# Performance work log

Measured on AMD Instinct MI355X. Metric: run time of the kernel, lower is better.

## Reference

```python
import jax, jax.numpy as jnp
import numpy as np

T, N, M, B = 512, 512, 256, 256

def setup_inputs() -> dict:
    key = jax.random.key(0)
    ks = jax.random.split(key, 6)
    h_t = jax.random.normal(ks[0], (1, B, M), dtype=jnp.float32)
    s_t = jax.random.normal(ks[1], (1, B, M), dtype=jnp.float32)
    data = jax.random.normal(ks[2], (B, T, N), dtype=jnp.float32)
    # torch Linear weight layout: (out_features, in_features)
    W_e = jax.random.normal(ks[3], (T, 2 * M), dtype=jnp.float32) / np.sqrt(2 * M)
    U_e = jax.random.normal(ks[4], (T, T), dtype=jnp.float32) / np.sqrt(T)
    v_e = jax.random.normal(ks[5], (1, T), dtype=jnp.float32) / np.sqrt(T)
    return {"h_t": h_t, "s_t": s_t, "data": data, "W_e": W_e, "U_e": U_e, "v_e": v_e}

def reference(h_t, s_t, data, W_e, U_e, v_e):
    # h_t, s_t: (1, B, m) -> (B, 2m); query is identical across the n repeats,
    # so project once and broadcast instead of materializing (B, n, 2m).
    query = jnp.concatenate([h_t[0], s_t[0]], axis=-1)          # (B, 2m)
    wq = query @ W_e.T                                          # (B, T)
    ud = jnp.einsum('btn,st->bns', data, U_e)                   # (B, n, T)
    alpha = jnp.tanh(wq[:, None, :] + ud)                       # (B, n, T)
    scores = jnp.einsum('bnt,t->bn', alpha, v_e[0])             # (B, n)
    attn = jax.nn.softmax(scores, axis=-1)[:, None, :]          # (B, 1, n)
    return attn
```

## Files before the change

### kernel.cpp

```cpp
#include <hip/hip_runtime.h>
#include <hip/hip_bf16.h>
#include <cmath>

#define T_DIM 512
#define N_DIM 512
#define M_DIM 256
#define B_DIM 256

typedef __bf16 bf16x8 __attribute__((ext_vector_type(8)));
typedef float  f32x4  __attribute__((ext_vector_type(4)));
typedef unsigned int u32;

__device__ __forceinline__ void gload16(const __bf16* g, __bf16* l) {
    __builtin_amdgcn_global_load_lds(
        (const __attribute__((address_space(1))) void*)g,
        (__attribute__((address_space(3))) void*)l, 16, 0, 0);
}

__device__ __forceinline__ int bkey(int r) { return ((r >> 3) ^ (r >> 1)) & 3; }

__device__ __forceinline__ u32 pack_trunc(float hi, float lo) {
    return __builtin_amdgcn_perm(__builtin_bit_cast(u32, hi),
                                 __builtin_bit_cast(u32, lo), 0x07060302u);
}

__device__ __forceinline__ float ftanh(float x) {
    return 1.f - 2.f / (__expf(2.f * x) + 1.f);
}

__global__ __launch_bounds__(256) void uconv_kernel(
    const float* __restrict__ U, __bf16* __restrict__ Uh)
{
    const int i = (blockIdx.x * 256 + threadIdx.x) * 2;
    float2 v = *(const float2*)(U + i);
    Uh[i]   = (__bf16)v.x;
    Uh[i+1] = (__bf16)v.y;
}

__global__ __launch_bounds__(256) void wq_kernel(
    const float* __restrict__ h_t, const float* __restrict__ s_t,
    const float* __restrict__ W_e, float* __restrict__ wq)
{
    __shared__ float q[2 * M_DIM];
    const int b = blockIdx.x;
    const int tid = threadIdx.x;
    q[tid]         = h_t[(size_t)b * M_DIM + tid];
    q[M_DIM + tid] = s_t[(size_t)b * M_DIM + tid];
    __syncthreads();
    for (int tt = tid; tt < T_DIM; tt += 256) {
        const float4* wrow = (const float4*)(W_e + (size_t)tt * (2 * M_DIM));
        float acc = 0.f;
        #pragma unroll 4
        for (int k4 = 0; k4 < (2 * M_DIM) / 4; ++k4) {
            float4 w = wrow[k4];
            acc += q[4*k4+0] * w.x + q[4*k4+1] * w.y
                 + q[4*k4+2] * w.z + q[4*k4+3] * w.w;
        }
        wq[(size_t)b * T_DIM + tt] = acc;
    }
}

__global__ __launch_bounds__(512, 2) void fused11_kernel(
    const float* __restrict__ data, const __bf16* __restrict__ Uh,
    const float* __restrict__ v_e, const float* __restrict__ wq,
    float* __restrict__ scores)
{
    __shared__ __align__(16) __bf16 As[2][128 * 32];
    __shared__ __align__(16) __bf16 Bs[2][512 * 32];
    __shared__ float sc2[4][128];

    const int wg   = blockIdx.x;
    const int bgrp = wg >> 2;
    const int nb   = wg & 3;

    const int tid  = threadIdx.x;
    const int lane = tid & 63;
    const int wid  = tid >> 6;
    const int wm   = wid >> 2;
    const int wn   = wid & 3;

    f32x4 acc[4][8];
    const f32x4 zero = {0.f, 0.f, 0.f, 0.f};
    #pragma unroll
    for (int i = 0; i < 4; ++i)
        #pragma unroll
        for (int j = 0; j < 8; ++j)
            acc[i][j] = zero;

    const int rp = tid >> 5;
    const int nq = tid & 31;
    const int n0 = nq * 4;

    const float* Apan = data + ((size_t)bgrp * 4 * T_DIM) * N_DIM + nb * 128 + n0;

    const __bf16* Bb = Uh;
    const int r0   = tid >> 2;
    const int keyB = bkey(r0);
    const int ce   = (((tid & 3) ^ keyB) * 8);

    const int fr = lane & 15;
    const int kb = (lane >> 4) * 8;

    int aoff[4];
    #pragma unroll
    for (int mi = 0; mi < 4; ++mi) {
        const int row = wm * 64 + mi * 16 + fr;
        aoff[mi] = row * 32 + (kb ^ (bkey(row) << 3));
    }
    int boff[8];
    #pragma unroll
    for (int ni = 0; ni < 8; ++ni) {
        const int row = wn * 128 + ni * 16 + fr;
        boff[ni] = row * 32 + (kb ^ (bkey(row) << 3));
    }

    float vev[8];
    #pragma unroll
    for (int ni = 0; ni < 8; ++ni)
        vev[ni] = v_e[wn * 128 + ni * 16 + fr];
    const int g = lane >> 4;

    float4 pa0, pa1;
    {
        const float* s0 = Apan + (size_t)(2 * rp) * N_DIM;
        pa0 = *(const float4*)s0;
        pa1 = *(const float4*)(s0 + N_DIM);
    }
    #pragma unroll
    for (int i = 0; i < 4; ++i)
        gload16(Bb + (size_t)(i * 128 + r0) * T_DIM + ce,
                &Bs[0][0] + (size_t)i * 128 * 32 + tid * 8);
    {
        u32* As32 = (u32*)As[0];
        const float lo_[4] = {pa0.x, pa0.y, pa0.z, pa0.w};
        const float hi_[4] = {pa1.x, pa1.y, pa1.z, pa1.w};
        #pragma unroll
        for (int j = 0; j < 4; ++j) {
            const u32 w = pack_trunc(hi_[j], lo_[j]);
            const int key = bkey(n0 + j);
            As32[(n0 + j) * 16 + (rp ^ (key << 2))] = w;
        }
    }
    {
        const float* sn = Apan + (size_t)(32 + 2 * rp) * N_DIM;
        pa0 = *(const float4*)sn;
        pa1 = *(const float4*)(sn + N_DIM);
    }
    __syncthreads();

    for (int t = 0; t < 64; ++t) {
        const int cur = t & 1;

        bf16x8 a[4], bv[8];
        #pragma unroll
        for (int mi = 0; mi < 4; ++mi)
            a[mi] = *(const bf16x8*)&As[cur][aoff[mi]];
        #pragma unroll
        for (int ni = 0; ni < 8; ++ni)
            bv[ni] = *(const bf16x8*)&Bs[cur][boff[ni]];

        if (t < 63) {
            const int nxt = cur ^ 1;
            const int kcol = ((t + 1) & 15) << 5;
            #pragma unroll
            for (int i = 0; i < 4; ++i)
                gload16(Bb + (size_t)(i * 128 + r0) * T_DIM + kcol + ce,
                        &Bs[nxt][0] + (size_t)i * 128 * 32 + tid * 8);
            u32* As32 = (u32*)As[nxt];
            const float lo_[4] = {pa0.x, pa0.y, pa0.z, pa0.w};
            const float hi_[4] = {pa1.x, pa1.y, pa1.z, pa1.w};
            #pragma unroll
            for (int j = 0; j < 4; ++j) {
                const u32 w = pack_trunc(hi_[j], lo_[j]);
                const int key = bkey(n0 + j);
                As32[(n0 + j) * 16 + (rp ^ (key << 2))] = w;
            }
            if (t < 62) {
                const float* sn = Apan + (size_t)(32 * (t + 2) + 2 * rp) * N_DIM;
                pa0 = *(const float4*)sn;
                pa1 = *(const float4*)(sn + N_DIM);
            }
        }

        __builtin_amdgcn_s_setprio(1);
        #pragma unroll
        for (int mi = 0; mi < 4; ++mi)
            #pragma unroll
            for (int ni = 0; ni < 8; ++ni)
                acc[mi][ni] = __builtin_amdgcn_mfma_f32_16x16x32_bf16(a[mi], bv[ni], acc[mi][ni], 0, 0, 0);
        __builtin_amdgcn_s_setprio(0);

        __syncthreads();

        if ((t & 15) == 15) {
            const int b = bgrp * 4 + (t >> 4);
            float wqv[8];
            #pragma unroll
            for (int ni = 0; ni < 8; ++ni)
                wqv[ni] = wq[(size_t)b * T_DIM + wn * 128 + ni * 16 + fr];
            #pragma unroll
            for (int mi = 0; mi < 4; ++mi) {
                #pragma unroll
                for (int rg = 0; rg < 4; ++rg) {
                    float part = 0.f;
                    #pragma unroll
                    for (int ni = 0; ni < 8; ++ni)
                        part += vev[ni] * ftanh(wqv[ni] + acc[mi][ni][rg]);
                    part += __shfl_xor(part, 1);
                    part += __shfl_xor(part, 2);
                    part += __shfl_xor(part, 4);
                    part += __shfl_xor(part, 8);
                    if (fr == 0)
                        sc2[wn][wm * 64 + mi * 16 + 4 * g + rg] = part;
                }
            }
            __syncthreads();
            if (tid < 128) {
                const float s = sc2[0][tid] + sc2[1][tid] + sc2[2][tid] + sc2[3][tid];
                scores[(size_t)b * N_DIM + nb * 128 + tid] = s;
            }
            if (t < 63) {
                #pragma unroll
                for (int i = 0; i < 4; ++i)
                    #pragma unroll
                    for (int j = 0; j < 8; ++j)
                        acc[i][j] = zero;
            }
        }
    }
}

__global__ __launch_bounds__(512) void softmax_kernel(
    const float* __restrict__ scores, float* __restrict__ out)
{
    const int b = blockIdx.x;
    const int n = threadIdx.x;
    float s = scores[(size_t)b * N_DIM + n];

    float m = s;
    #pragma unroll
    for (int off = 1; off < 64; off <<= 1)
        m = fmaxf(m, __shfl_xor(m, off));
    __shared__ float red[8];
    const int wv = n >> 6;
    if ((n & 63) == 0) red[wv] = m;
    __syncthreads();
    float bm = red[0];
    #pragma unroll
    for (int i = 1; i < 8; ++i) bm = fmaxf(bm, red[i]);

    float e = expf(s - bm);
    float t = e;
    #pragma unroll
    for (int off = 1; off < 64; off <<= 1)
        t += __shfl_xor(t, off);
    __syncthreads();
    if ((n & 63) == 0) red[wv] = t;
    __syncthreads();
    float tot = 0.f;
    #pragma unroll
    for (int i = 0; i < 8; ++i) tot += red[i];

    out[(size_t)b * N_DIM + n] = e / tot;
}

extern "C" void kernel_launch(void* const* d_in, const int* in_sizes, int n_in,
                              void* d_out, int out_size, void* d_ws, size_t ws_size,
                              hipStream_t stream) {
    const float* h_t  = (const float*)d_in[0];
    const float* s_t  = (const float*)d_in[1];
    const float* data = (const float*)d_in[2];
    const float* W_e  = (const float*)d_in[3];
    const float* U_e  = (const float*)d_in[4];
    const float* v_e  = (const float*)d_in[5];
    float* out = (float*)d_out;

    const size_t wq_elems     = (size_t)B_DIM * T_DIM;
    const size_t score_elems  = (size_t)B_DIM * N_DIM;
    const size_t u_elems      = (size_t)T_DIM * T_DIM;

    float* wq      = (float*)d_ws;
    float* scores  = wq + wq_elems;
    __bf16* Uh     = (__bf16*)(scores + score_elems);

    wq_kernel<<<B_DIM, 256, 0, stream>>>(h_t, s_t, W_e, wq);
    uconv_kernel<<<(int)(u_elems / 512), 256, 0, stream>>>(U_e, Uh);
    fused11_kernel<<<256, 512, 0, stream>>>(data, Uh, v_e, wq, scores);
    softmax_kernel<<<B_DIM, 512, 0, stream>>>(scores, out);
}
```

Baseline: 162.1 us.

## Triple-buffer U tiles with prefetch distance two and explicit vmcnt waits

```diff
diff --git a/kernel.cpp b/kernel.cpp
--- a/kernel.cpp
+++ b/kernel.cpp
@@ -10,6 +10,11 @@
 typedef __bf16 bf16x8 __attribute__((ext_vector_type(8)));
 typedef float  f32x4  __attribute__((ext_vector_type(4)));
 typedef unsigned int u32;
+
+#define WAITVM(N) asm volatile("s_waitcnt vmcnt(" #N ") lgkmcnt(0)" ::: "memory")
+#define FENCED_BARRIER() do { __builtin_amdgcn_sched_barrier(0); \
+                              __builtin_amdgcn_s_barrier();      \
+                              __builtin_amdgcn_sched_barrier(0); } while (0)
 
 __device__ __forceinline__ void gload16(const __bf16* g, __bf16* l) {
     __builtin_amdgcn_global_load_lds(
@@ -60,13 +65,13 @@
     }
 }
 
-__global__ __launch_bounds__(512, 2) void fused11_kernel(
+__global__ __launch_bounds__(512, 2) void fused12_kernel(
     const float* __restrict__ data, const __bf16* __restrict__ Uh,
     const float* __restrict__ v_e, const float* __restrict__ wq,
     float* __restrict__ scores)
 {
     __shared__ __align__(16) __bf16 As[2][128 * 32];
-    __shared__ __align__(16) __bf16 Bs[2][512 * 32];
+    __shared__ __align__(16) __bf16 Bs[3][512 * 32];
     __shared__ float sc2[4][128];
 
     const int wg   = blockIdx.x;
@@ -90,13 +95,11 @@
     const int rp = tid >> 5;
     const int nq = tid & 31;
     const int n0 = nq * 4;
-
     const float* Apan = data + ((size_t)bgrp * 4 * T_DIM) * N_DIM + nb * 128 + n0;
 
     const __bf16* Bb = Uh;
     const int r0   = tid >> 2;
-    const int keyB = bkey(r0);
-    const int ce   = (((tid & 3) ^ keyB) * 8);
+    const int ce   = (((tid & 3) ^ bkey(r0)) * 8);
 
     const int fr = lane & 15;
     const int kb = (lane >> 4) * 8;
@@ -121,113 +124,127 @@
     const int g = lane >> 4;
 
     float4 pa0, pa1;
-    {
-        const float* s0 = Apan + (size_t)(2 * rp) * N_DIM;
-        pa0 = *(const float4*)s0;
-        pa1 = *(const float4*)(s0 + N_DIM);
-    }
-    #pragma unroll
-    for (int i = 0; i < 4; ++i)
-        gload16(Bb + (size_t)(i * 128 + r0) * T_DIM + ce,
-                &Bs[0][0] + (size_t)i * 128 * 32 + tid * 8);
-    {
-        u32* As32 = (u32*)As[0];
-        const float lo_[4] = {pa0.x, pa0.y, pa0.z, pa0.w};
-        const float hi_[4] = {pa1.x, pa1.y, pa1.z, pa1.w};
-        #pragma unroll
-        for (int j = 0; j < 4; ++j) {
-            const u32 w = pack_trunc(hi_[j], lo_[j]);
-            const int key = bkey(n0 + j);
-            As32[(n0 + j) * 16 + (rp ^ (key << 2))] = w;
-        }
-    }
-    {
-        const float* sn = Apan + (size_t)(32 + 2 * rp) * N_DIM;
-        pa0 = *(const float4*)sn;
-        pa1 = *(const float4*)(sn + N_DIM);
-    }
-    __syncthreads();
-
-    for (int t = 0; t < 64; ++t) {
-        const int cur = t & 1;
-
-        bf16x8 a[4], bv[8];
-        #pragma unroll
-        for (int mi = 0; mi < 4; ++mi)
-            a[mi] = *(const bf16x8*)&As[cur][aoff[mi]];
-        #pragma unroll
-        for (int ni = 0; ni < 8; ++ni)
-            bv[ni] = *(const bf16x8*)&Bs[cur][boff[ni]];
-
-        if (t < 63) {
-            const int nxt = cur ^ 1;
-            const int kcol = ((t + 1) & 15) << 5;
-            #pragma unroll
-            for (int i = 0; i < 4; ++i)
-                gload16(Bb + (size_t)(i * 128 + r0) * T_DIM + kcol + ce,
-                        &Bs[nxt][0] + (size_t)i * 128 * 32 + tid * 8);
-            u32* As32 = (u32*)As[nxt];
-            const float lo_[4] = {pa0.x, pa0.y, pa0.z, pa0.w};
-            const float hi_[4] = {pa1.x, pa1.y, pa1.z, pa1.w};
-            #pragma unroll
-            for (int j = 0; j < 4; ++j) {
-                const u32 w = pack_trunc(hi_[j], lo_[j]);
-                const int key = bkey(n0 + j);
-                As32[(n0 + j) * 16 + (rp ^ (key << 2))] = w;
-            }
-            if (t < 62) {
-                const float* sn = Apan + (size_t)(32 * (t + 2) + 2 * rp) * N_DIM;
-                pa0 = *(const float4*)sn;
-                pa1 = *(const float4*)(sn + N_DIM);
-            }
-        }
-
-        __builtin_amdgcn_s_setprio(1);
-        #pragma unroll
-        for (int mi = 0; mi < 4; ++mi)
-            #pragma unroll
-            for (int ni = 0; ni < 8; ++ni)
-                acc[mi][ni] = __builtin_amdgcn_mfma_f32_16x16x32_bf16(a[mi], bv[ni], acc[mi][ni], 0, 0, 0);
-        __builtin_amdgcn_s_setprio(0);
-
-        __syncthreads();
-
-        if ((t & 15) == 15) {
-            const int b = bgrp * 4 + (t >> 4);
-            float wqv[8];
-            #pragma unroll
-            for (int ni = 0; ni < 8; ++ni)
-                wqv[ni] = wq[(size_t)b * T_DIM + wn * 128 + ni * 16 + fr];
-            #pragma unroll
-            for (int mi = 0; mi < 4; ++mi) {
-                #pragma unroll
-                for (int rg = 0; rg < 4; ++rg) {
-                    float part = 0.f;
-                    #pragma unroll
-                    for (int ni = 0; ni < 8; ++ni)
-                        part += vev[ni] * ftanh(wqv[ni] + acc[mi][ni][rg]);
-                    part += __shfl_xor(part, 1);
-                    part += __shfl_xor(part, 2);
-                    part += __shfl_xor(part, 4);
-                    part += __shfl_xor(part, 8);
-                    if (fr == 0)
-                        sc2[wn][wm * 64 + mi * 16 + 4 * g + rg] = part;
-                }
-            }
-            __syncthreads();
-            if (tid < 128) {
-                const float s = sc2[0][tid] + sc2[1][tid] + sc2[2][tid] + sc2[3][tid];
-                scores[(size_t)b * N_DIM + nb * 128 + tid] = s;
-            }
-            if (t < 63) {
-                #pragma unroll
-                for (int i = 0; i < 4; ++i)
-                    #pragma unroll
-                    for (int j = 0; j < 8; ++j)
-                        acc[i][j] = zero;
-            }
-        }
-    }
+
+#define CVT_STORE(DST)                                                        \
+    {                                                                         \
+        u32* As32_ = (u32*)(DST);                                             \
+        const float lo_[4] = {pa0.x, pa0.y, pa0.z, pa0.w};                    \
+        const float hi_[4] = {pa1.x, pa1.y, pa1.z, pa1.w};                    \
+        _Pragma("unroll")                                                     \
+        for (int j = 0; j < 4; ++j) {                                         \
+            const u32 w_ = pack_trunc(hi_[j], lo_[j]);                        \
+            const int key_ = bkey(n0 + j);                                    \
+            As32_[(n0 + j) * 16 + (rp ^ (key_ << 2))] = w_;                   \
+        }                                                                     \
+    }
+
+#define LOAD_PA(T)                                                            \
+    {                                                                         \
+        const float* sn_ = Apan + (size_t)(32 * (T) + 2 * rp) * N_DIM;        \
+        pa0 = *(const float4*)sn_;                                            \
+        pa1 = *(const float4*)(sn_ + N_DIM);                                  \
+    }
+
+#define STAGE_B(T, RING)                                                      \
+    {                                                                         \
+        const int kcol_ = ((T) & 15) << 5;                                    \
+        _Pragma("unroll")                                                     \
+        for (int i = 0; i < 4; ++i)                                           \
+            gload16(Bb + (size_t)(i * 128 + r0) * T_DIM + kcol_ + ce,         \
+                    &Bs[RING][0] + (size_t)i * 128 * 32 + tid * 8);           \
+    }
+
+#define K_STEP(K, CURA, RINGC, RINGS, MODE)                                   \
+    {                                                                         \
+        bf16x8 a_[4], bv_[8];                                                 \
+        _Pragma("unroll")                                                     \
+        for (int mi = 0; mi < 4; ++mi)                                        \
+            a_[mi] = *(const bf16x8*)&As[CURA][aoff[mi]];                     \
+        _Pragma("unroll")                                                     \
+        for (int ni = 0; ni < 8; ++ni)                                        \
+            bv_[ni] = *(const bf16x8*)&Bs[RINGC][boff[ni]];                   \
+        if ((MODE) <= 1) CVT_STORE(As[(CURA) ^ 1]);                           \
+        if ((MODE) == 0) { LOAD_PA((K) + 2); STAGE_B((K) + 2, RINGS); }       \
+        __builtin_amdgcn_s_setprio(1);                                        \
+        _Pragma("unroll")                                                     \
+        for (int mi = 0; mi < 4; ++mi)                                        \
+            _Pragma("unroll")                                                 \
+            for (int ni = 0; ni < 8; ++ni)                                    \
+                acc[mi][ni] = __builtin_amdgcn_mfma_f32_16x16x32_bf16(        \
+                    a_[mi], bv_[ni], acc[mi][ni], 0, 0, 0);                   \
+        __builtin_amdgcn_s_setprio(0);                                        \
+        if ((MODE) == 0)      { WAITVM(6); FENCED_BARRIER(); }                \
+        else if ((MODE) == 1) { WAITVM(0); FENCED_BARRIER(); }                \
+    }
+
+#define PANEL_EPI(BIDX, DORESET)                                              \
+    {                                                                         \
+        const int b_ = bgrp * 4 + (BIDX);                                     \
+        float wqv_[8];                                                        \
+        _Pragma("unroll")                                                     \
+        for (int ni = 0; ni < 8; ++ni)                                        \
+            wqv_[ni] = wq[(size_t)b_ * T_DIM + wn * 128 + ni * 16 + fr];      \
+        _Pragma("unroll")                                                     \
+        for (int mi = 0; mi < 4; ++mi) {                                      \
+            _Pragma("unroll")                                                 \
+            for (int rg = 0; rg < 4; ++rg) {                                  \
+                float part_ = 0.f;                                            \
+                _Pragma("unroll")                                             \
+                for (int ni = 0; ni < 8; ++ni)                                \
+                    part_ += vev[ni] * ftanh(wqv_[ni] + acc[mi][ni][rg]);     \
+                part_ += __shfl_xor(part_, 1);                                \
+                part_ += __shfl_xor(part_, 2);                                \
+                part_ += __shfl_xor(part_, 4);                                \
+                part_ += __shfl_xor(part_, 8);                                \
+                if (fr == 0)                                                  \
+                    sc2[wn][wm * 64 + mi * 16 + 4 * g + rg] = part_;          \
+            }                                                                 \
+        }                                                                     \
+        asm volatile("s_waitcnt lgkmcnt(0)" ::: "memory");                    \
+        FENCED_BARRIER();                                                     \
+        if (tid < 128) {                                                      \
+            const float s_ = sc2[0][tid] + sc2[1][tid]                        \
+                           + sc2[2][tid] + sc2[3][tid];                       \
+            scores[(size_t)b_ * N_DIM + nb * 128 + tid] = s_;                 \
+        }                                                                     \
+        if (DORESET) {                                                        \
+            _Pragma("unroll")                                                 \
+            for (int i = 0; i < 4; ++i)                                       \
+                _Pragma("unroll")                                             \
+                for (int j = 0; j < 8; ++j)                                   \
+                    acc[i][j] = zero;                                         \
+        }                                                                     \
+    }
+
+    LOAD_PA(0);
+    CVT_STORE(As[0]);
+    STAGE_B(0, 0);
+    LOAD_PA(1);
+    STAGE_B(1, 1);
+    WAITVM(6);
+    FENCED_BARRIER();
+
+    for (int m = 0; m < 10; ++m) {
+        const int k6 = 6 * m;
+        K_STEP(k6 + 0, 0, 0, 2, 0); if (((k6 + 0) & 15) == 15) PANEL_EPI((k6 + 0) >> 4, 1);
+        K_STEP(k6 + 1, 1, 1, 0, 0); if (((k6 + 1) & 15) == 15) PANEL_EPI((k6 + 1) >> 4, 1);
+        K_STEP(k6 + 2, 0, 2, 1, 0); if (((k6 + 2) & 15) == 15) PANEL_EPI((k6 + 2) >> 4, 1);
+        K_STEP(k6 + 3, 1, 0, 2, 0); if (((k6 + 3) & 15) == 15) PANEL_EPI((k6 + 3) >> 4, 1);
+        K_STEP(k6 + 4, 0, 1, 0, 0); if (((k6 + 4) & 15) == 15) PANEL_EPI((k6 + 4) >> 4, 1);
+        K_STEP(k6 + 5, 1, 2, 1, 0); if (((k6 + 5) & 15) == 15) PANEL_EPI((k6 + 5) >> 4, 1);
+    }
+
+    K_STEP(60, 0, 0, 2, 0);
+    K_STEP(61, 1, 1, 0, 0);
+    K_STEP(62, 0, 2, 0, 1);
+    K_STEP(63, 1, 0, 0, 2);
+    PANEL_EPI(3, 0);
+
+#undef K_STEP
+#undef PANEL_EPI
+#undef CVT_STORE
+#undef LOAD_PA
+#undef STAGE_B
 }
 
 __global__ __launch_bounds__(512) void softmax_kernel(
@@ -285,6 +302,6 @@
 
     wq_kernel<<<B_DIM, 256, 0, stream>>>(h_t, s_t, W_e, wq);
     uconv_kernel<<<(int)(u_elems / 512), 256, 0, stream>>>(U_e, Uh);
-    fused11_kernel<<<256, 512, 0, stream>>>(data, Uh, v_e, wq, scores);
+    fused12_kernel<<<256, 512, 0, stream>>>(data, Uh, v_e, wq, scores);
     softmax_kernel<<<B_DIM, 512, 0, stream>>>(scores, out);
 }
```

Result: faster. 157.3 us, median of 2 (-3.0%).
